# Optimization experiments

Measured on AMD Instinct MI355X. Metric: run time of the kernel, lower is better.

The kernel has to match this reference:

```python
import jax, jax.numpy as jnp
import numpy as np


def setup_inputs() -> dict:
    key = jax.random.key(0)
    k1, k2, k3, k4 = jax.random.split(key, 4)
    N, M, D = 4096, 4096, 1024
    H = jax.random.normal(k1, (N, D), dtype=jnp.float32)
    K = jax.random.normal(k2, (M, D), dtype=jnp.float32)
    V = jax.random.normal(k3, (M, D), dtype=jnp.float32)
    attn_mask = jax.random.uniform(k4, (N, M), dtype=jnp.float32)
    return {"H": H, "K": K, "V": V, "attn_mask": attn_mask}


def reference(H, K, V, attn_mask):
    # scores: [N, M] = H @ K^T, scaled by sqrt(d)
    d = H.shape[1]
    scores = jnp.matmul(H, K.T) / jnp.sqrt(jnp.asarray(d, dtype=H.dtype))
    # double softmax with elementwise mask multiply in between
    probs = jax.nn.softmax(jax.nn.softmax(scores, axis=1) * attn_mask, axis=1)
    return jnp.matmul(probs, V)
```

## Files before the change

kernel.cpp:

```cpp
#include <hip/hip_runtime.h>
#include <cstdint>

typedef unsigned short u16;
typedef __bf16 bf16x8 __attribute__((ext_vector_type(8)));
typedef float f32x4 __attribute__((ext_vector_type(4)));

__device__ __forceinline__ float bf2f(u16 h) {
  union { unsigned int u; float f; } v; v.u = ((unsigned int)h) << 16; return v.f;
}
__device__ __forceinline__ u16 f2bf(float f) {
  union { float f; unsigned int u; } v; v.f = f;
  unsigned int u = v.u;
  return (u16)((u + 0x7FFFu + ((u >> 16) & 1u)) >> 16);
}

__device__ __forceinline__ void ld_lds16(const void* g, void* l) {
  __builtin_amdgcn_global_load_lds(
      (const __attribute__((address_space(1))) unsigned int*)g,
      (__attribute__((address_space(3))) unsigned int*)l, 16, 0, 0);
}

template <int MODE>
__global__ __launch_bounds__(256, 2) void gemm_kernel(
    const u16* __restrict__ A, const u16* __restrict__ B,
    void* __restrict__ Cout, float* __restrict__ L1,
    const float* __restrict__ L2, int ldA, int ldB, int ldC)
{
  __shared__ u16 As[128 * 64];
  __shared__ u16 Bs[128 * 64];

  const int tid  = threadIdx.x;
  const int lane = tid & 63;
  const int w    = tid >> 6;
  const int wr   = w >> 1;
  const int wc   = w & 1;
  const int quad = lane >> 4;
  const int cIn  = lane & 15;

  const int flat = blockIdx.x;
  const int xcd  = flat & 7;
  const int i    = flat >> 3;
  int rowBlk, colBlk, kb, ke;
  if (MODE == 0) {
    rowBlk = ((xcd >> 2) * 16 + (i & 15)) * 128;
    colBlk = ((xcd & 3) * 8 + (i >> 4)) * 128;
    kb = 0; ke = 1024;
  } else {
    rowBlk = (((xcd & 1) * 16) + (i & 15)) * 128;
    colBlk = (i >> 4) * 128;
    kb = (xcd >> 1) * 1024; ke = kb + 1024;
  }

  const int lrow   = lane >> 3;
  const int gchunk = (lane & 7) ^ lrow;

  f32x4 acc[4][4];
  #pragma unroll
  for (int a = 0; a < 4; ++a)
    #pragma unroll
    for (int b = 0; b < 4; ++b) acc[a][b] = {0.f, 0.f, 0.f, 0.f};

  for (int k0 = kb; k0 < ke; k0 += 64) {
    #pragma unroll
    for (int t = 0; t < 4; ++t) {
      int rg = w * 4 + t;
      const u16* ga = A + (size_t)(rowBlk + rg * 8 + lrow) * ldA + k0 + gchunk * 8;
      const u16* gb = B + (size_t)(colBlk + rg * 8 + lrow) * ldB + k0 + gchunk * 8;
      ld_lds16(ga, &As[rg * 512]);
      ld_lds16(gb, &Bs[rg * 512]);
    }
    __syncthreads();

    #pragma unroll
    for (int ks = 0; ks < 2; ++ks) {
      bf16x8 af[4], bfr[4];
      #pragma unroll
      for (int mi = 0; mi < 4; ++mi) {
        int row = wr * 64 + mi * 16 + cIn;
        int ch  = (ks * 4 + quad) ^ (row & 7);
        af[mi]  = *(const bf16x8*)&As[row * 64 + ch * 8];
      }
      #pragma unroll
      for (int ni = 0; ni < 4; ++ni) {
        int row = wc * 64 + ni * 16 + cIn;
        int ch  = (ks * 4 + quad) ^ (row & 7);
        bfr[ni] = *(const bf16x8*)&Bs[row * 64 + ch * 8];
      }
      #pragma unroll
      for (int mi = 0; mi < 4; ++mi)
        #pragma unroll
        for (int ni = 0; ni < 4; ++ni)
          acc[mi][ni] = __builtin_amdgcn_mfma_f32_16x16x32_bf16(
              af[mi], bfr[ni], acc[mi][ni], 0, 0, 0);
    }
    __syncthreads();
  }

  if (MODE == 0) {
    u16* S = (u16*)Cout;
    const float scale = 0.03125f;
    #pragma unroll
    for (int mi = 0; mi < 4; ++mi) {
      float rs[4] = {0.f, 0.f, 0.f, 0.f};
      #pragma unroll
      for (int ni = 0; ni < 4; ++ni) {
        int col = colBlk + wc * 64 + ni * 16 + cIn;
        #pragma unroll
        for (int r = 0; r < 4; ++r) {
          int row = rowBlk + wr * 64 + mi * 16 + quad * 4 + r;
          u16 sb = f2bf(acc[mi][ni][r] * scale);
          S[(size_t)row * ldC + col] = sb;
          rs[r] += __expf(bf2f(sb));
        }
      }
      #pragma unroll
      for (int m = 1; m < 16; m <<= 1)
        #pragma unroll
        for (int r = 0; r < 4; ++r) rs[r] += __shfl_xor(rs[r], m, 64);
      if (cIn == 0) {
        #pragma unroll
        for (int r = 0; r < 4; ++r)
          atomicAdd(&L1[rowBlk + wr * 64 + mi * 16 + quad * 4 + r], rs[r]);
      }
    }
  } else {
    float* Out = (float*)Cout;
    #pragma unroll
    for (int mi = 0; mi < 4; ++mi) {
      #pragma unroll
      for (int r = 0; r < 4; ++r) {
        int row   = rowBlk + wr * 64 + mi * 16 + quad * 4 + r;
        float inv = 1.0f / L2[row];
        #pragma unroll
        for (int ni = 0; ni < 4; ++ni) {
          int col = colBlk + wc * 64 + ni * 16 + cIn;
          atomicAdd(&Out[(size_t)row * ldC + col], acc[mi][ni][r] * inv);
        }
      }
    }
  }
}

__global__ __launch_bounds__(256) void prep_kernel(
    const float* __restrict__ H, const float* __restrict__ Kin,
    const float* __restrict__ V, u16* __restrict__ Hb, u16* __restrict__ Kb,
    u16* __restrict__ Vt)
{
  int b = blockIdx.x;
  if (b < 8192) {
    const float* src = (b < 4096) ? H : Kin;
    u16* dst = (b < 4096) ? Hb : Kb;
    int i = (b & 4095) * 256 + threadIdx.x;
    float4 v = ((const float4*)src)[i];
    ushort4 o;
    o.x = f2bf(v.x); o.y = f2bf(v.y); o.z = f2bf(v.z); o.w = f2bf(v.w);
    ((ushort4*)dst)[i] = o;
  } else {
    __shared__ float tile[32][33];
    b -= 8192;
    int c0 = (b & 31) * 32;
    int r0 = (b >> 5) * 32;
    int tx = threadIdx.x & 31, ty = threadIdx.x >> 5;
    #pragma unroll
    for (int s = 0; s < 32; s += 8)
      tile[ty + s][tx] = V[(size_t)(r0 + ty + s) * 1024 + c0 + tx];
    __syncthreads();
    #pragma unroll
    for (int s = 0; s < 32; s += 8)
      Vt[(size_t)(c0 + ty + s) * 4096 + r0 + tx] = f2bf(tile[tx][ty + s]);
  }
}

__global__ __launch_bounds__(256) void softmax2_kernel(
    u16* __restrict__ S, const float* __restrict__ mask,
    const float* __restrict__ L1, float* __restrict__ L2, int M)
{
  int row = blockIdx.x;
  float inv = 1.0f / L1[row];
  u16* srow = S + (size_t)row * M;
  const float* mrow = mask + (size_t)row * M;
  float lsum = 0.f;
  for (int base = threadIdx.x * 16; base < M; base += blockDim.x * 16) {
    u16 sl[16];
    *(uint4*)(sl)     = *(const uint4*)(srow + base);
    *(uint4*)(sl + 8) = *(const uint4*)(srow + base + 8);
    float mv[16];
    #pragma unroll
    for (int q = 0; q < 4; ++q)
      *(float4*)(mv + q * 4) = *(const float4*)(mrow + base + q * 4);
    #pragma unroll
    for (int j = 0; j < 16; ++j) {
      float t = __expf(bf2f(sl[j])) * inv * mv[j];
      float p = __expf(t);
      lsum += p;
      sl[j] = f2bf(p);
    }
    *(uint4*)(srow + base)     = *(uint4*)(sl);
    *(uint4*)(srow + base + 8) = *(uint4*)(sl + 8);
  }
  #pragma unroll
  for (int m = 1; m < 64; m <<= 1) lsum += __shfl_xor(lsum, m, 64);
  __shared__ float wred[4];
  if ((threadIdx.x & 63) == 0) wred[threadIdx.x >> 6] = lsum;
  __syncthreads();
  if (threadIdx.x == 0) L2[row] = wred[0] + wred[1] + wred[2] + wred[3];
}

extern "C" void kernel_launch(void* const* d_in, const int* in_sizes, int n_in,
                              void* d_out, int out_size, void* d_ws, size_t ws_size,
                              hipStream_t stream) {
  const float* H    = (const float*)d_in[0];
  const float* Kin  = (const float*)d_in[1];
  const float* V    = (const float*)d_in[2];
  const float* mask = (const float*)d_in[3];
  float* out = (float*)d_out;

  const int N = 4096, M = 4096, D = 1024;

  char* ws = (char*)d_ws;
  u16*   Hb = (u16*)(ws);
  u16*   Kb = (u16*)(ws + (8ull << 20));
  u16*   Vt = (u16*)(ws + (16ull << 20));
  u16*   S  = (u16*)(ws + (24ull << 20));
  float* L1 = (float*)(ws + (56ull << 20));
  float* L2 = (float*)(ws + (56ull << 20) + 16384);

  hipMemsetAsync(L1, 0, 32768, stream);
  hipMemsetAsync(out, 0, (size_t)N * D * sizeof(float), stream);

  prep_kernel<<<dim3(12288), dim3(256), 0, stream>>>(H, Kin, V, Hb, Kb, Vt);

  gemm_kernel<0><<<dim3(1024), dim3(256), 0, stream>>>(
      Hb, Kb, S, L1, nullptr, D, D, M);
  softmax2_kernel<<<dim3(N), dim3(256), 0, stream>>>(S, mask, L1, L2, M);
  gemm_kernel<1><<<dim3(1024), dim3(256), 0, stream>>>(
      S, Vt, out, nullptr, L2, M, M, D);
}
```

Baseline: 260.3 us.

## Drop split-K atomics in second GEMM, stage score stores via LDS, fold memsets

The second GEMM no longer splits K four ways with float atomicAdd into a zeroed output. It now uses 64x128 tiles over the full K=4096 and writes results directly with nontemporal stores, which removes the 16 MB output memset and the atomic traffic. The first GEMM epilogue stages the bf16 scores in padded LDS and writes coalesced 16-byte nontemporal rows instead of scattered 2-byte stores. The L1 zeroing moves into an extra block of the prep kernel, and the mask load becomes nontemporal. Trade-off: the second GEMM has only 512 blocks doing long K loops, so parallelism is lower, and the __launch_bounds__ occupancy hint was dropped.

```diff
diff --git a/kernel.cpp b/kernel.cpp
--- a/kernel.cpp
+++ b/kernel.cpp
@@ -4,6 +4,7 @@
 typedef unsigned short u16;
 typedef __bf16 bf16x8 __attribute__((ext_vector_type(8)));
 typedef float f32x4 __attribute__((ext_vector_type(4)));
+typedef unsigned int u32x4 __attribute__((ext_vector_type(4)));
 
 __device__ __forceinline__ float bf2f(u16 h) {
   union { unsigned int u; float f; } v; v.u = ((unsigned int)h) << 16; return v.f;
@@ -20,14 +21,13 @@
       (__attribute__((address_space(3))) unsigned int*)l, 16, 0, 0);
 }
 
-template <int MODE>
-__global__ __launch_bounds__(256, 2) void gemm_kernel(
+__global__ __launch_bounds__(256) void gemm1_kernel(
     const u16* __restrict__ A, const u16* __restrict__ B,
-    void* __restrict__ Cout, float* __restrict__ L1,
-    const float* __restrict__ L2, int ldA, int ldB, int ldC)
+    u16* __restrict__ S, float* __restrict__ L1, int ldA, int ldB, int ldC)
 {
-  __shared__ u16 As[128 * 64];
-  __shared__ u16 Bs[128 * 64];
+  __shared__ u16 smem[128 * 136];
+  u16* As = smem;
+  u16* Bs = smem + 8192;
 
   const int tid  = threadIdx.x;
   const int lane = tid & 63;
@@ -40,16 +40,8 @@
   const int flat = blockIdx.x;
   const int xcd  = flat & 7;
   const int i    = flat >> 3;
-  int rowBlk, colBlk, kb, ke;
-  if (MODE == 0) {
-    rowBlk = ((xcd >> 2) * 16 + (i & 15)) * 128;
-    colBlk = ((xcd & 3) * 8 + (i >> 4)) * 128;
-    kb = 0; ke = 1024;
-  } else {
-    rowBlk = (((xcd & 1) * 16) + (i & 15)) * 128;
-    colBlk = (i >> 4) * 128;
-    kb = (xcd >> 1) * 1024; ke = kb + 1024;
-  }
+  const int rowBlk = ((xcd >> 2) * 16 + (i & 15)) * 128;
+  const int colBlk = ((xcd & 3) * 8 + (i >> 4)) * 128;
 
   const int lrow   = lane >> 3;
   const int gchunk = (lane & 7) ^ lrow;
@@ -60,7 +52,7 @@
     #pragma unroll
     for (int b = 0; b < 4; ++b) acc[a][b] = {0.f, 0.f, 0.f, 0.f};
 
-  for (int k0 = kb; k0 < ke; k0 += 64) {
+  for (int k0 = 0; k0 < 1024; k0 += 64) {
     #pragma unroll
     for (int t = 0; t < 4; ++t) {
       int rg = w * 4 + t;
@@ -96,46 +88,125 @@
     __syncthreads();
   }
 
-  if (MODE == 0) {
-    u16* S = (u16*)Cout;
-    const float scale = 0.03125f;
-    #pragma unroll
-    for (int mi = 0; mi < 4; ++mi) {
-      float rs[4] = {0.f, 0.f, 0.f, 0.f};
+  const float scale = 0.03125f;
+  #pragma unroll
+  for (int mi = 0; mi < 4; ++mi) {
+    float rs[4] = {0.f, 0.f, 0.f, 0.f};
+    #pragma unroll
+    for (int ni = 0; ni < 4; ++ni) {
+      int colT = wc * 64 + ni * 16 + cIn;
+      #pragma unroll
+      for (int r = 0; r < 4; ++r) {
+        int rowT = wr * 64 + mi * 16 + quad * 4 + r;
+        u16 sb = f2bf(acc[mi][ni][r] * scale);
+        smem[rowT * 136 + colT] = sb;
+        rs[r] += __expf(bf2f(sb));
+      }
+    }
+    #pragma unroll
+    for (int m = 1; m < 16; m <<= 1)
+      #pragma unroll
+      for (int r = 0; r < 4; ++r) rs[r] += __shfl_xor(rs[r], m, 64);
+    if (cIn == 0) {
+      #pragma unroll
+      for (int r = 0; r < 4; ++r)
+        atomicAdd(&L1[rowBlk + wr * 64 + mi * 16 + quad * 4 + r], rs[r]);
+    }
+  }
+  __syncthreads();
+  #pragma unroll
+  for (int it = 0; it < 8; ++it) {
+    int j  = it * 256 + tid;
+    int r  = j >> 4;
+    int c8 = j & 15;
+    u32x4 v = *(const u32x4*)&smem[r * 136 + c8 * 8];
+    __builtin_nontemporal_store(
+        v, (u32x4*)&S[(size_t)(rowBlk + r) * ldC + colBlk + c8 * 8]);
+  }
+}
+
+__global__ __launch_bounds__(256) void gemm2_kernel(
+    const u16* __restrict__ A, const u16* __restrict__ B,
+    float* __restrict__ Out, const float* __restrict__ L2,
+    int ldA, int ldB, int ldC)
+{
+  __shared__ u16 As[64 * 64];
+  __shared__ u16 Bs[128 * 64];
+
+  const int tid  = threadIdx.x;
+  const int lane = tid & 63;
+  const int w    = tid >> 6;
+  const int wrow = w >> 1;
+  const int wcol = w & 1;
+  const int quad = lane >> 4;
+  const int cIn  = lane & 15;
+
+  const int flat = blockIdx.x;
+  const int xcd  = flat & 7;
+  const int i    = flat >> 3;
+  const int rowBlk = (xcd * 8 + (i & 7)) * 64;
+  const int colBlk = (i >> 3) * 128;
+
+  const int lrow   = lane >> 3;
+  const int gchunk = (lane & 7) ^ lrow;
+
+  f32x4 acc[2][4];
+  #pragma unroll
+  for (int a = 0; a < 2; ++a)
+    #pragma unroll
+    for (int b = 0; b < 4; ++b) acc[a][b] = {0.f, 0.f, 0.f, 0.f};
+
+  for (int k0 = 0; k0 < 4096; k0 += 64) {
+    #pragma unroll
+    for (int t = 0; t < 2; ++t) {
+      int rg = w * 2 + t;
+      const u16* ga = A + (size_t)(rowBlk + rg * 8 + lrow) * ldA + k0 + gchunk * 8;
+      ld_lds16(ga, &As[rg * 512]);
+    }
+    #pragma unroll
+    for (int t = 0; t < 4; ++t) {
+      int rg = w * 4 + t;
+      const u16* gb = B + (size_t)(colBlk + rg * 8 + lrow) * ldB + k0 + gchunk * 8;
+      ld_lds16(gb, &Bs[rg * 512]);
+    }
+    __syncthreads();
+
+    #pragma unroll
+    for (int ks = 0; ks < 2; ++ks) {
+      bf16x8 af[2], bfr[4];
+      #pragma unroll
+      for (int mi = 0; mi < 2; ++mi) {
+        int row = wrow * 32 + mi * 16 + cIn;
+        int ch  = (ks * 4 + quad) ^ (row & 7);
+        af[mi]  = *(const bf16x8*)&As[row * 64 + ch * 8];
+      }
       #pragma unroll
       for (int ni = 0; ni < 4; ++ni) {
-        int col = colBlk + wc * 64 + ni * 16 + cIn;
+        int row = wcol * 64 + ni * 16 + cIn;
+        int ch  = (ks * 4 + quad) ^ (row & 7);
+        bfr[ni] = *(const bf16x8*)&Bs[row * 64 + ch * 8];
+      }
+      #pragma unroll
+      for (int mi = 0; mi < 2; ++mi)
         #pragma unroll
-        for (int r = 0; r < 4; ++r) {
-          int row = rowBlk + wr * 64 + mi * 16 + quad * 4 + r;
-          u16 sb = f2bf(acc[mi][ni][r] * scale);
-          S[(size_t)row * ldC + col] = sb;
-          rs[r] += __expf(bf2f(sb));
-        }
-      }
-      #pragma unroll
-      for (int m = 1; m < 16; m <<= 1)
-        #pragma unroll
-        for (int r = 0; r < 4; ++r) rs[r] += __shfl_xor(rs[r], m, 64);
-      if (cIn == 0) {
-        #pragma unroll
-        for (int r = 0; r < 4; ++r)
-          atomicAdd(&L1[rowBlk + wr * 64 + mi * 16 + quad * 4 + r], rs[r]);
-      }
-    }
-  } else {
-    float* Out = (float*)Cout;
-    #pragma unroll
-    for (int mi = 0; mi < 4; ++mi) {
-      #pragma unroll
-      for (int r = 0; r < 4; ++r) {
-        int row   = rowBlk + wr * 64 + mi * 16 + quad * 4 + r;
-        float inv = 1.0f / L2[row];
-        #pragma unroll
-        for (int ni = 0; ni < 4; ++ni) {
-          int col = colBlk + wc * 64 + ni * 16 + cIn;
-          atomicAdd(&Out[(size_t)row * ldC + col], acc[mi][ni][r] * inv);
-        }
+        for (int ni = 0; ni < 4; ++ni)
+          acc[mi][ni] = __builtin_amdgcn_mfma_f32_16x16x32_bf16(
+              af[mi], bfr[ni], acc[mi][ni], 0, 0, 0);
+    }
+    __syncthreads();
+  }
+
+  #pragma unroll
+  for (int mi = 0; mi < 2; ++mi) {
+    #pragma unroll
+    for (int r = 0; r < 4; ++r) {
+      int row   = rowBlk + wrow * 32 + mi * 16 + quad * 4 + r;
+      float inv = 1.0f / L2[row];
+      #pragma unroll
+      for (int ni = 0; ni < 4; ++ni) {
+        int col = colBlk + wcol * 64 + ni * 16 + cIn;
+        __builtin_nontemporal_store(acc[mi][ni][r] * inv,
+                                    &Out[(size_t)row * ldC + col]);
       }
     }
   }
@@ -144,7 +215,7 @@
 __global__ __launch_bounds__(256) void prep_kernel(
     const float* __restrict__ H, const float* __restrict__ Kin,
     const float* __restrict__ V, u16* __restrict__ Hb, u16* __restrict__ Kb,
-    u16* __restrict__ Vt)
+    u16* __restrict__ Vt, float* __restrict__ L1)
 {
   int b = blockIdx.x;
   if (b < 8192) {
@@ -155,7 +226,7 @@
     ushort4 o;
     o.x = f2bf(v.x); o.y = f2bf(v.y); o.z = f2bf(v.z); o.w = f2bf(v.w);
     ((ushort4*)dst)[i] = o;
-  } else {
+  } else if (b < 12288) {
     __shared__ float tile[32][33];
     b -= 8192;
     int c0 = (b & 31) * 32;
@@ -168,6 +239,11 @@
     #pragma unroll
     for (int s = 0; s < 32; s += 8)
       Vt[(size_t)(c0 + ty + s) * 4096 + r0 + tx] = f2bf(tile[tx][ty + s]);
+  } else {
+    float4* z = (float4*)L1;
+    #pragma unroll
+    for (int q = 0; q < 8; ++q)
+      z[q * 256 + threadIdx.x] = {0.f, 0.f, 0.f, 0.f};
   }
 }
 
@@ -187,7 +263,8 @@
     float mv[16];
     #pragma unroll
     for (int q = 0; q < 4; ++q)
-      *(float4*)(mv + q * 4) = *(const float4*)(mrow + base + q * 4);
+      *(f32x4*)(mv + q * 4) =
+          __builtin_nontemporal_load((const f32x4*)(mrow + base + q * 4));
     #pragma unroll
     for (int j = 0; j < 16; ++j) {
       float t = __expf(bf2f(sl[j])) * inv * mv[j];
@@ -225,14 +302,11 @@
   float* L1 = (float*)(ws + (56ull << 20));
   float* L2 = (float*)(ws + (56ull << 20) + 16384);
 
-  hipMemsetAsync(L1, 0, 32768, stream);
-  hipMemsetAsync(out, 0, (size_t)N * D * sizeof(float), stream);
-
-  prep_kernel<<<dim3(12288), dim3(256), 0, stream>>>(H, Kin, V, Hb, Kb, Vt);
-
-  gemm_kernel<0><<<dim3(1024), dim3(256), 0, stream>>>(
-      Hb, Kb, S, L1, nullptr, D, D, M);
+  prep_kernel<<<dim3(12289), dim3(256), 0, stream>>>(H, Kin, V, Hb, Kb, Vt, L1);
+
+  gemm1_kernel<<<dim3(1024), dim3(256), 0, stream>>>(Hb, Kb, S, L1, D, D, M);
+
   softmax2_kernel<<<dim3(N), dim3(256), 0, stream>>>(S, mask, L1, L2, M);
-  gemm_kernel<1><<<dim3(1024), dim3(256), 0, stream>>>(
-      S, Vt, out, nullptr, L2, M, M, D);
-}
+
+  gemm2_kernel<<<dim3(512), dim3(256), 0, stream>>>(S, Vt, out, L2, M, M, D);
+}
```

After: 255.4 us. No clear change (-1.9%).
